# Performance work log

Hardware: AMD Instinct MI355X
Metric: run time of the kernel (lower is better)

The kernel has to match this reference:

```python
import jax, jax.numpy as jnp
import numpy as np

HIDDEN = 768
HEADS = 12
HEAD_DIM = HIDDEN // HEADS

def setup_inputs() -> dict:
    key = jax.random.key(0)
    ks = jax.random.split(key, 9)
    s = 1.0 / np.sqrt(HIDDEN)
    x = jax.random.normal(ks[0], (2, 2048, HIDDEN), dtype=jnp.float32)
    Wq = jax.random.normal(ks[1], (HIDDEN, HIDDEN), dtype=jnp.float32) * s
    bq = jnp.zeros((HIDDEN,), dtype=jnp.float32)
    Wk = jax.random.normal(ks[2], (HIDDEN, HIDDEN), dtype=jnp.float32) * s
    bk = jnp.zeros((HIDDEN,), dtype=jnp.float32)
    Wv = jax.random.normal(ks[3], (HIDDEN, HIDDEN), dtype=jnp.float32) * s
    bv = jnp.zeros((HIDDEN,), dtype=jnp.float32)
    Wo = jax.random.normal(ks[4], (HIDDEN, HIDDEN), dtype=jnp.float32) * s
    bo = jnp.zeros((HIDDEN,), dtype=jnp.float32)
    return {"x": x, "Wq": Wq, "bq": bq, "Wk": Wk, "bk": bk,
            "Wv": Wv, "bv": bv, "Wo": Wo, "bo": bo}

def reference(x, Wq, bq, Wk, bk, Wv, bv, Wo, bo):
    B, S, _ = x.shape
    # project and split heads: [B, H, S, D]
    def proj(W, b):
        return (x @ W + b).reshape(B, S, HEADS, HEAD_DIM).transpose(0, 2, 1, 3)
    q = proj(Wq, bq)
    k = proj(Wk, bk)
    v = proj(Wv, bv)
    # NOTE: original module does NOT scale by 1/sqrt(head_dim)
    scores = jnp.einsum('bhqd,bhkd->bhqk', q, k)
    attn = jax.nn.softmax(scores, axis=-1)
    out = jnp.einsum('bhqk,bhkd->bhqd', attn, v)
    out = out.transpose(0, 2, 1, 3).reshape(B, S, HIDDEN)
    return out @ Wo + bo
```

## Files before the change

kernel.cpp:

```cpp
#include <hip/hip_runtime.h>
#include <cstddef>

#define HIDDEN 768
#define NHEADS 12
#define HDIM   64
#define BATCH  2
#define SEQ    2048
#define NROWS  (BATCH*SEQ)
#define LOG2E  1.4426950408889634f

typedef float f32x4  __attribute__((ext_vector_type(4)));
typedef float f32x16 __attribute__((ext_vector_type(16)));
typedef short bf16x8 __attribute__((ext_vector_type(8)));

__device__ __forceinline__ float fast_exp2(float x){
    return __builtin_amdgcn_exp2f(x);
}

__device__ __forceinline__ unsigned short f2bf(float f){
    unsigned u = __builtin_bit_cast(unsigned, f);
    u = u + 0x7FFFu + ((u >> 16) & 1u);
    return (unsigned short)(u >> 16);
}
__device__ __forceinline__ unsigned packbf2(float a, float b){
    unsigned ua = (__builtin_bit_cast(unsigned, a) + 0x8000u) >> 16;
    unsigned ub = (__builtin_bit_cast(unsigned, b) + 0x8000u) & 0xFFFF0000u;
    return ua | ub;
}

__device__ __forceinline__ void gl_lds16(const unsigned short* g, unsigned short* l){
    __builtin_amdgcn_global_load_lds(
        (const __attribute__((address_space(1))) unsigned int*)g,
        (__attribute__((address_space(3))) unsigned int*)l, 16, 0, 0);
}

__global__ __launch_bounds__(256) void cvt_bf16(const float* __restrict__ in,
                                                unsigned short* __restrict__ out,
                                                int n4)
{
    const int i = blockIdx.x * 256 + threadIdx.x;
    if (i >= n4) return;
    const float4 v = reinterpret_cast<const float4*>(in)[i];
    ushort4 o;
    o.x = f2bf(v.x); o.y = f2bf(v.y); o.z = f2bf(v.z); o.w = f2bf(v.w);
    reinterpret_cast<ushort4*>(out)[i] = o;
}

__global__ __launch_bounds__(256) void transpose_cvt(const float* __restrict__ W,
                                                     unsigned short* __restrict__ Wt)
{
    __shared__ unsigned short t[64][66];
    const int k0 = blockIdx.y * 64, n0 = blockIdx.x * 64;
    const int row = threadIdx.x >> 2;
    const int c0  = (threadIdx.x & 3) * 16;
#pragma unroll
    for (int j = 0; j < 16; j += 4) {
        const float4 v = *reinterpret_cast<const float4*>(&W[(size_t)(k0 + row) * HIDDEN + n0 + c0 + j]);
        t[row][c0 + j + 0] = f2bf(v.x);
        t[row][c0 + j + 1] = f2bf(v.y);
        t[row][c0 + j + 2] = f2bf(v.z);
        t[row][c0 + j + 3] = f2bf(v.w);
    }
    __syncthreads();
#pragma unroll
    for (int j = 0; j < 16; j += 4) {
        ushort4 o;
        o.x = t[c0 + j + 0][row];
        o.y = t[c0 + j + 1][row];
        o.z = t[c0 + j + 2][row];
        o.w = t[c0 + j + 3][row];
        *reinterpret_cast<ushort4*>(&Wt[(size_t)(n0 + row) * HIDDEN + k0 + c0 + j]) = o;
    }
}

__global__ __launch_bounds__(256) void gemm_mfma(const unsigned short* __restrict__ A,
                                                 const unsigned short* __restrict__ Wt,
                                                 const float* __restrict__ bias,
                                                 void* __restrict__ Cout, int mode,
                                                 float scale)
{
    __shared__ unsigned short As[64 * 64];
    __shared__ unsigned short Bs[96 * 64];
    const int tid = threadIdx.x;
    const int l = tid & 63, w = tid >> 6;
    const int wm = w >> 1, wn = w & 1;
    const int l15 = l & 15, lg = l >> 4;
    const int srow = l >> 3, sslot = l & 7;
    const int m0 = blockIdx.y * 64, n0 = blockIdx.x * 96;

    f32x4 acc[2][3] = {};

    for (int k0 = 0; k0 < HIDDEN; k0 += 64) {
        __syncthreads();
#pragma unroll
        for (int a = 0; a < 2; ++a) {
            const int row = (a * 4 + w) * 8 + srow;
            const int sl = sslot ^ (row & 7);
            gl_lds16(&A[(size_t)(m0 + row) * HIDDEN + k0 + sl * 8], &As[(a * 4 + w) * 512]);
        }
#pragma unroll
        for (int b = 0; b < 3; ++b) {
            const int row = (b * 4 + w) * 8 + srow;
            const int sl = sslot ^ (row & 7);
            gl_lds16(&Wt[(size_t)(n0 + row) * HIDDEN + k0 + sl * 8], &Bs[(b * 4 + w) * 512]);
        }
        __syncthreads();

#pragma unroll
        for (int kk = 0; kk < 2; ++kk) {
            bf16x8 af[2], bfr[3];
#pragma unroll
            for (int mi = 0; mi < 2; ++mi) {
                const int r = wm * 32 + mi * 16 + l15;
                af[mi] = *reinterpret_cast<const bf16x8*>(&As[r * 64 + ((lg * 8 + kk * 32) ^ ((r & 7) << 3))]);
            }
#pragma unroll
            for (int ni = 0; ni < 3; ++ni) {
                const int r = wn * 48 + ni * 16 + l15;
                bfr[ni] = *reinterpret_cast<const bf16x8*>(&Bs[r * 64 + ((lg * 8 + kk * 32) ^ ((r & 7) << 3))]);
            }
#pragma unroll
            for (int mi = 0; mi < 2; ++mi)
#pragma unroll
                for (int ni = 0; ni < 3; ++ni)
                    acc[mi][ni] = __builtin_amdgcn_mfma_f32_16x16x32_bf16(af[mi], bfr[ni], acc[mi][ni], 0, 0, 0);
        }
    }

#pragma unroll
    for (int mi = 0; mi < 2; ++mi) {
#pragma unroll
        for (int ni = 0; ni < 3; ++ni) {
#pragma unroll
            for (int rr = 0; rr < 4; ++rr) {
                const int row = m0 + wm * 32 + mi * 16 + lg * 4 + rr;
                const int col = n0 + wn * 48 + ni * 16 + l15;
                const float v = (acc[mi][ni][rr] + bias[col]) * scale;
                if (mode == 0) {
                    const int b = row >> 11, s = row & (SEQ - 1);
                    const int hh = col >> 6, d = col & (HDIM - 1);
                    ((unsigned short*)Cout)[(((size_t)b * NHEADS + hh) * SEQ + s) * HDIM + d] = f2bf(v);
                } else if (mode == 1) {
                    const int b = row >> 11, s = row & (SEQ - 1);
                    const int hh = col >> 6, d = col & (HDIM - 1);
                    ((unsigned short*)Cout)[(((size_t)b * NHEADS + hh) * HDIM + d) * SEQ + s] = f2bf(v);
                } else {
                    ((float*)Cout)[(size_t)row * HIDDEN + col] = v;
                }
            }
        }
    }
}

__global__ __launch_bounds__(256) void attn_mfma(const unsigned short* __restrict__ Q,
                                                 const unsigned short* __restrict__ K,
                                                 const unsigned short* __restrict__ Vt,
                                                 unsigned short* __restrict__ O)
{
    __shared__ __align__(16) char shraw[33792];
    unsigned short* Ks  = (unsigned short*)shraw;
    unsigned short* Vs  = (unsigned short*)(shraw + 16384);
    float*          xch = (float*)shraw;
    unsigned int*   Ep  = (unsigned int*)(shraw + 16384);
    float2*         mlx = (float2*)(shraw + 32768);

    const int tid = threadIdx.x;
    const int l = tid & 63;
    const int wq2 = (tid >> 6) & 1;
    const int wkv = tid >> 7;
    const int l31 = l & 31, hi = l >> 5;
    const int lr = l >> 3, slot = l & 7;
    const int q0 = blockIdx.x * 64;
    const int h = blockIdx.y, b = blockIdx.z;
    const size_t base = ((size_t)b * NHEADS + h) * (size_t)SEQ * HDIM;

    const int q = q0 + wq2 * 32 + l31;
    bf16x8 qf[4];
#pragma unroll
    for (int t = 0; t < 4; ++t)
        qf[t] = *reinterpret_cast<const bf16x8*>(&Q[base + (size_t)q * HDIM + 16 * t + 8 * hi]);

    f32x16 accO[2] = {};
    float m = -1e30f, lsum = 0.f;

    unsigned short* Kb = Ks + wkv * 4096;
    unsigned short* Vb = Vs + wkv * 4096;
    const int kvbase = wkv * (SEQ / 2);

    for (int i = 0; i < SEQ / 128; ++i) {
        const int t0 = kvbase + i * 64;
        __syncthreads();
#pragma unroll
        for (int j = 0; j < 4; ++j) {
            const int row = (j * 2 + wq2) * 8 + lr;
            const int sl = slot ^ (row & 7);
            gl_lds16(&K [base + (size_t)(t0 + row) * HDIM + sl * 8], &Kb[(j * 2 + wq2) * 512]);
            gl_lds16(&Vt[base + (size_t)row * SEQ + t0 + sl * 8],    &Vb[(j * 2 + wq2) * 512]);
        }
        __syncthreads();

        f32x16 s0v = {}, s1v = {};
#pragma unroll
        for (int t = 0; t < 4; ++t) {
            const int co = 16 * t + 8 * hi;
            const int r0 = l31, r1 = 32 + l31;
            const bf16x8 k0 = *reinterpret_cast<const bf16x8*>(&Kb[r0 * 64 + (co ^ ((r0 & 7) << 3))]);
            const bf16x8 k1 = *reinterpret_cast<const bf16x8*>(&Kb[r1 * 64 + (co ^ ((r1 & 7) << 3))]);
            s0v = __builtin_amdgcn_mfma_f32_32x32x16_bf16(k0, qf[t], s0v, 0, 0, 0);
            s1v = __builtin_amdgcn_mfma_f32_32x32x16_bf16(k1, qf[t], s1v, 0, 0, 0);
        }

        float tmax = s0v[0];
#pragma unroll
        for (int r = 1; r < 16; ++r) tmax = fmaxf(tmax, s0v[r]);
#pragma unroll
        for (int r = 0; r < 16; ++r) tmax = fmaxf(tmax, s1v[r]);
        tmax = fmaxf(tmax, __shfl_xor(tmax, 32));

        if (tmax > m + 8.f) {
            const float scl = fast_exp2(m - tmax);
            lsum *= scl;
#pragma unroll
            for (int r = 0; r < 16; ++r) { accO[0][r] *= scl; accO[1][r] *= scl; }
            m = tmax;
        }

        unsigned wv[16];
        float ls = 0.f;
#pragma unroll
        for (int a = 0; a < 8; ++a) {
            const float pa = fast_exp2(s0v[2 * a] - m);
            const float pb = fast_exp2(s0v[2 * a + 1] - m);
            ls += pa + pb;
            wv[a] = packbf2(pa, pb);
        }
#pragma unroll
        for (int a = 0; a < 8; ++a) {
            const float pa = fast_exp2(s1v[2 * a] - m);
            const float pb = fast_exp2(s1v[2 * a + 1] - m);
            ls += pa + pb;
            wv[8 + a] = packbf2(pa, pb);
        }
        ls += __shfl_xor(ls, 32);
        lsum += ls;

#pragma unroll
        for (int slot2 = 0; slot2 < 4; ++slot2) {
            const unsigned w0 = wv[slot2 * 4 + 0], w1 = wv[slot2 * 4 + 1];
            const unsigned w2 = wv[slot2 * 4 + 2], w3 = wv[slot2 * 4 + 3];
            const unsigned x0 = (unsigned)__shfl_xor((int)w0, 32);
            const unsigned x1 = (unsigned)__shfl_xor((int)w1, 32);
            const unsigned x2 = (unsigned)__shfl_xor((int)w2, 32);
            const unsigned x3 = (unsigned)__shfl_xor((int)w3, 32);
            uint4 fr;
            fr.x = hi ? x2 : w0;
            fr.y = hi ? x3 : w1;
            fr.z = hi ? w2 : x0;
            fr.w = hi ? w3 : x1;
            const bf16x8 pfrag = __builtin_bit_cast(bf16x8, fr);
#pragma unroll
            for (int db = 0; db < 2; ++db) {
                const int vr = 32 * db + l31;
                const int co = (16 * slot2 + 8 * hi) ^ ((vr & 7) << 3);
                const bf16x8 vf = *reinterpret_cast<const bf16x8*>(&Vb[vr * 64 + co]);
                accO[db] = __builtin_amdgcn_mfma_f32_32x32x16_bf16(vf, pfrag, accO[db], 0, 0, 0);
            }
        }
    }

    __syncthreads();
    if (!hi) mlx[(wq2 * 2 + wkv) * 32 + l31] = make_float2(m, lsum);
    __syncthreads();
    const float2 mp = mlx[(wq2 * 2 + (1 - wkv)) * 32 + l31];
    const float M  = fmaxf(m, mp.x);
    const float s  = fast_exp2(m - M);
    const float lf = lsum * s + mp.y * fast_exp2(mp.x - M);

    if (wkv == 1) {
#pragma unroll
        for (int db = 0; db < 2; ++db)
#pragma unroll
            for (int r = 0; r < 16; ++r) {
                const int d = 32 * db + (r & 3) + 8 * (r >> 2) + 4 * hi;
                xch[wq2 * 2048 + d * 32 + l31] = accO[db][r] * s;
            }
    }
    __syncthreads();
    if (wkv == 0) {
        const float inv = 1.f / lf;
#pragma unroll
        for (int db = 0; db < 2; ++db)
#pragma unroll
            for (int r = 0; r < 16; ++r) {
                const int d = 32 * db + (r & 3) + 8 * (r >> 2) + 4 * hi;
                accO[db][r] = (accO[db][r] * s + xch[wq2 * 2048 + d * 32 + l31]) * inv;
            }
#pragma unroll
        for (int db = 0; db < 2; ++db)
#pragma unroll
            for (int a = 0; a < 8; ++a) {
                const unsigned wd = packbf2(accO[db][2 * a], accO[db][2 * a + 1]);
                const int pi = 16 * db + 4 * (a >> 1) + (a & 1) + 2 * hi;
                Ep[(wq2 * 32 + l31) * 33 + pi] = wd;
            }
    }
    __syncthreads();
    if (wkv == 0) {
#pragma unroll
        for (int pss = 0; pss < 4; ++pss) {
            const int idx = pss * 64 + l;
            const int qr = idx >> 3, c = idx & 7;
            uint4 ov;
            ov.x = Ep[(wq2 * 32 + qr) * 33 + c * 4 + 0];
            ov.y = Ep[(wq2 * 32 + qr) * 33 + c * 4 + 1];
            ov.z = Ep[(wq2 * 32 + qr) * 33 + c * 4 + 2];
            ov.w = Ep[(wq2 * 32 + qr) * 33 + c * 4 + 3];
            *reinterpret_cast<uint4*>(&O[((size_t)b * SEQ + q0 + wq2 * 32 + qr) * HIDDEN + h * HDIM + c * 8]) = ov;
        }
    }
}

extern "C" void kernel_launch(void* const* d_in, const int* in_sizes, int n_in,
                              void* d_out, int out_size, void* d_ws, size_t ws_size,
                              hipStream_t stream)
{
    const float* x  = (const float*)d_in[0];
    const float* Wq = (const float*)d_in[1];
    const float* bq = (const float*)d_in[2];
    const float* Wk = (const float*)d_in[3];
    const float* bk = (const float*)d_in[4];
    const float* Wv = (const float*)d_in[5];
    const float* bv = (const float*)d_in[6];
    const float* Wo = (const float*)d_in[7];
    const float* bo = (const float*)d_in[8];
    float* out = (float*)d_out;

    unsigned short* p = (unsigned short*)d_ws;
    const size_t szX = (size_t)NROWS * HIDDEN;
    const size_t szW = (size_t)HIDDEN * HIDDEN;
    const size_t szH = (size_t)BATCH * NHEADS * SEQ * HDIM;
    unsigned short* xb  = p;              p += szX;
    unsigned short* Wqt = p;              p += szW;
    unsigned short* Wkt = p;              p += szW;
    unsigned short* Wvt = p;              p += szW;
    unsigned short* Wot = p;              p += szW;
    unsigned short* Qb  = p;              p += szH;
    unsigned short* Kb  = p;              p += szH;
    unsigned short* Vtb = p;              p += szH;
    unsigned short* Oab = p;              p += szX;

    cvt_bf16<<<(int)(szX / 4 + 255) / 256, 256, 0, stream>>>(x, xb, (int)(szX / 4));
    dim3 tg(HIDDEN / 64, HIDDEN / 64);
    transpose_cvt<<<tg, 256, 0, stream>>>(Wq, Wqt);
    transpose_cvt<<<tg, 256, 0, stream>>>(Wk, Wkt);
    transpose_cvt<<<tg, 256, 0, stream>>>(Wv, Wvt);
    transpose_cvt<<<tg, 256, 0, stream>>>(Wo, Wot);

    dim3 gg(HIDDEN / 96, NROWS / 64);
    gemm_mfma<<<gg, 256, 0, stream>>>(xb, Wqt, bq, Qb, 0, LOG2E);
    gemm_mfma<<<gg, 256, 0, stream>>>(xb, Wkt, bk, Kb, 0, 1.0f);
    gemm_mfma<<<gg, 256, 0, stream>>>(xb, Wvt, bv, Vtb, 1, 1.0f);

    attn_mfma<<<dim3(SEQ / 64, NHEADS, BATCH), 256, 0, stream>>>(Qb, Kb, Vtb, Oab);

    gemm_mfma<<<gg, 256, 0, stream>>>(Oab, Wot, bo, out, 2, 1.0f);
}
```

Before: 130.7 us.

## Batch weight transposes and QKV GEMMs into single launches, tune attention inner loop

Merges the four weight transpose launches into one grid using blockIdx.z, and the three QKV projection GEMMs into one launch, which cuts launch overhead and lets the GPU fill more CUs at once. In the attention kernel it raises wave priority around the MFMA sections, computes the row max as a tree reduction, and replaces manual bf16 packing with the v_cvt_pk_bf16_f32 instruction. The hardware convert rounds to nearest even rather than round-half-up, so probabilities can differ slightly. The setprio hints may not help scheduling.

```diff
diff --git a/kernel.cpp b/kernel.cpp
--- a/kernel.cpp
+++ b/kernel.cpp
@@ -27,6 +27,11 @@
     unsigned ub = (__builtin_bit_cast(unsigned, b) + 0x8000u) & 0xFFFF0000u;
     return ua | ub;
 }
+__device__ __forceinline__ unsigned cvtpk_bf16(float a, float b){
+    unsigned r;
+    asm("v_cvt_pk_bf16_f32 %0, %1, %2" : "=v"(r) : "v"(a), "v"(b));
+    return r;
+}
 
 __device__ __forceinline__ void gl_lds16(const unsigned short* g, unsigned short* l){
     __builtin_amdgcn_global_load_lds(
@@ -46,9 +51,19 @@
     reinterpret_cast<ushort4*>(out)[i] = o;
 }
 
-__global__ __launch_bounds__(256) void transpose_cvt(const float* __restrict__ W,
-                                                     unsigned short* __restrict__ Wt)
-{
+__global__ __launch_bounds__(256) void transpose_cvt4(const float* __restrict__ W0,
+                                                      const float* __restrict__ W1,
+                                                      const float* __restrict__ W2,
+                                                      const float* __restrict__ W3,
+                                                      unsigned short* __restrict__ T0,
+                                                      unsigned short* __restrict__ T1,
+                                                      unsigned short* __restrict__ T2,
+                                                      unsigned short* __restrict__ T3)
+{
+    const int z = blockIdx.z;
+    const float* W = (z == 0) ? W0 : (z == 1) ? W1 : (z == 2) ? W2 : W3;
+    unsigned short* Wt = (z == 0) ? T0 : (z == 1) ? T1 : (z == 2) ? T2 : T3;
+
     __shared__ unsigned short t[64][66];
     const int k0 = blockIdx.y * 64, n0 = blockIdx.x * 64;
     const int row = threadIdx.x >> 2;
@@ -73,14 +88,13 @@
     }
 }
 
-__global__ __launch_bounds__(256) void gemm_mfma(const unsigned short* __restrict__ A,
-                                                 const unsigned short* __restrict__ Wt,
-                                                 const float* __restrict__ bias,
-                                                 void* __restrict__ Cout, int mode,
-                                                 float scale)
-{
-    __shared__ unsigned short As[64 * 64];
-    __shared__ unsigned short Bs[96 * 64];
+__device__ __forceinline__ void gemm_body(const unsigned short* __restrict__ A,
+                                          const unsigned short* __restrict__ Wt,
+                                          const float* __restrict__ bias,
+                                          void* __restrict__ Cout, int mode,
+                                          float scale,
+                                          unsigned short* As, unsigned short* Bs)
+{
     const int tid = threadIdx.x;
     const int l = tid & 63, w = tid >> 6;
     const int wm = w >> 1, wn = w & 1;
@@ -152,6 +166,38 @@
     }
 }
 
+__global__ __launch_bounds__(256) void qkv_gemm(const unsigned short* __restrict__ A,
+                                                const unsigned short* __restrict__ Wqt,
+                                                const unsigned short* __restrict__ Wkt,
+                                                const unsigned short* __restrict__ Wvt,
+                                                const float* __restrict__ bq,
+                                                const float* __restrict__ bk,
+                                                const float* __restrict__ bv,
+                                                unsigned short* __restrict__ Qb,
+                                                unsigned short* __restrict__ Kb,
+                                                unsigned short* __restrict__ Vtb)
+{
+    __shared__ unsigned short As[64 * 64];
+    __shared__ unsigned short Bs[96 * 64];
+    const int z = blockIdx.z;
+    const unsigned short* Wt = (z == 0) ? Wqt : (z == 1) ? Wkt : Wvt;
+    const float* bias = (z == 0) ? bq : (z == 1) ? bk : bv;
+    void* out = (z == 0) ? (void*)Qb : (z == 1) ? (void*)Kb : (void*)Vtb;
+    const int mode = (z == 2) ? 1 : 0;
+    const float scale = (z == 0) ? LOG2E : 1.0f;
+    gemm_body(A, Wt, bias, out, mode, scale, As, Bs);
+}
+
+__global__ __launch_bounds__(256) void out_gemm(const unsigned short* __restrict__ A,
+                                                const unsigned short* __restrict__ Wt,
+                                                const float* __restrict__ bias,
+                                                float* __restrict__ Cout)
+{
+    __shared__ unsigned short As[64 * 64];
+    __shared__ unsigned short Bs[96 * 64];
+    gemm_body(A, Wt, bias, Cout, 2, 1.0f, As, Bs);
+}
+
 __global__ __launch_bounds__(256) void attn_mfma(const unsigned short* __restrict__ Q,
                                                  const unsigned short* __restrict__ K,
                                                  const unsigned short* __restrict__ Vt,
@@ -200,6 +246,7 @@
         __syncthreads();
 
         f32x16 s0v = {}, s1v = {};
+        __builtin_amdgcn_s_setprio(1);
 #pragma unroll
         for (int t = 0; t < 4; ++t) {
             const int co = 16 * t + 8 * hi;
@@ -209,12 +256,14 @@
             s0v = __builtin_amdgcn_mfma_f32_32x32x16_bf16(k0, qf[t], s0v, 0, 0, 0);
             s1v = __builtin_amdgcn_mfma_f32_32x32x16_bf16(k1, qf[t], s1v, 0, 0, 0);
         }
-
-        float tmax = s0v[0];
-#pragma unroll
-        for (int r = 1; r < 16; ++r) tmax = fmaxf(tmax, s0v[r]);
-#pragma unroll
-        for (int r = 0; r < 16; ++r) tmax = fmaxf(tmax, s1v[r]);
+        __builtin_amdgcn_s_setprio(0);
+
+        float tmax = -1e30f;
+#pragma unroll
+        for (int r = 0; r < 16; r += 4) {
+            tmax = fmaxf(tmax, fmaxf(fmaxf(s0v[r], s0v[r + 1]), fmaxf(s0v[r + 2], s0v[r + 3])));
+            tmax = fmaxf(tmax, fmaxf(fmaxf(s1v[r], s1v[r + 1]), fmaxf(s1v[r + 2], s1v[r + 3])));
+        }
         tmax = fmaxf(tmax, __shfl_xor(tmax, 32));
 
         if (tmax > m + 8.f) {
@@ -232,14 +281,14 @@
             const float pa = fast_exp2(s0v[2 * a] - m);
             const float pb = fast_exp2(s0v[2 * a + 1] - m);
             ls += pa + pb;
-            wv[a] = packbf2(pa, pb);
+            wv[a] = cvtpk_bf16(pa, pb);
         }
 #pragma unroll
         for (int a = 0; a < 8; ++a) {
             const float pa = fast_exp2(s1v[2 * a] - m);
             const float pb = fast_exp2(s1v[2 * a + 1] - m);
             ls += pa + pb;
-            wv[8 + a] = packbf2(pa, pb);
+            wv[8 + a] = cvtpk_bf16(pa, pb);
         }
         ls += __shfl_xor(ls, 32);
         lsum += ls;
@@ -258,6 +307,7 @@
             fr.z = hi ? w2 : x0;
             fr.w = hi ? w3 : x1;
             const bf16x8 pfrag = __builtin_bit_cast(bf16x8, fr);
+            __builtin_amdgcn_s_setprio(1);
 #pragma unroll
             for (int db = 0; db < 2; ++db) {
                 const int vr = 32 * db + l31;
@@ -265,6 +315,7 @@
                 const bf16x8 vf = *reinterpret_cast<const bf16x8*>(&Vb[vr * 64 + co]);
                 accO[db] = __builtin_amdgcn_mfma_f32_32x32x16_bf16(vf, pfrag, accO[db], 0, 0, 0);
             }
+            __builtin_amdgcn_s_setprio(0);
         }
     }
 
@@ -350,18 +401,13 @@
     unsigned short* Oab = p;              p += szX;
 
     cvt_bf16<<<(int)(szX / 4 + 255) / 256, 256, 0, stream>>>(x, xb, (int)(szX / 4));
-    dim3 tg(HIDDEN / 64, HIDDEN / 64);
-    transpose_cvt<<<tg, 256, 0, stream>>>(Wq, Wqt);
-    transpose_cvt<<<tg, 256, 0, stream>>>(Wk, Wkt);
-    transpose_cvt<<<tg, 256, 0, stream>>>(Wv, Wvt);
-    transpose_cvt<<<tg, 256, 0, stream>>>(Wo, Wot);
-
-    dim3 gg(HIDDEN / 96, NROWS / 64);
-    gemm_mfma<<<gg, 256, 0, stream>>>(xb, Wqt, bq, Qb, 0, LOG2E);
-    gemm_mfma<<<gg, 256, 0, stream>>>(xb, Wkt, bk, Kb, 0, 1.0f);
-    gemm_mfma<<<gg, 256, 0, stream>>>(xb, Wvt, bv, Vtb, 1, 1.0f);
+    transpose_cvt4<<<dim3(HIDDEN / 64, HIDDEN / 64, 4), 256, 0, stream>>>(
+        Wq, Wk, Wv, Wo, Wqt, Wkt, Wvt, Wot);
+
+    qkv_gemm<<<dim3(HIDDEN / 96, NROWS / 64, 3), 256, 0, stream>>>(
+        xb, Wqt, Wkt, Wvt, bq, bk, bv, Qb, Kb, Vtb);
 
     attn_mfma<<<dim3(SEQ / 64, NHEADS, BATCH), 256, 0, stream>>>(Qb, Kb, Vtb, Oab);
 
-    gemm_mfma<<<gg, 256, 0, stream>>>(Oab, Wot, bo, out, 2, 1.0f);
-}
+    out_gemm<<<dim3(HIDDEN / 96, NROWS / 64), 256, 0, stream>>>(Oab, Wot, bo, out);
+}
```

Result: faster. 112.1 us (median of 2 runs) (-14.2%).
